# Optimization experiments

Hardware: AMD Instinct MI355X
Metric: run time of the kernel (lower is better)

## Reference

```python
import jax, jax.numpy as jnp
import numpy as np


def bilinear_resize(x, out_h, out_w):
    # x: [B, C, H, W]; matches torch F.interpolate(mode='bilinear', align_corners=False)
    B, C, H, W = x.shape
    ry = jnp.clip((jnp.arange(out_h, dtype=jnp.float32) + 0.5) * (H / out_h) - 0.5, 0.0, H - 1)
    rx = jnp.clip((jnp.arange(out_w, dtype=jnp.float32) + 0.5) * (W / out_w) - 0.5, 0.0, W - 1)
    y0 = jnp.floor(ry).astype(jnp.int32); y1 = jnp.minimum(y0 + 1, H - 1)
    x0 = jnp.floor(rx).astype(jnp.int32); x1 = jnp.minimum(x0 + 1, W - 1)
    wy = (ry - y0)[:, None]  # [out_h,1]
    wx = (rx - x0)[None, :]  # [1,out_w]
    r0 = x[:, :, y0, :]; r1 = x[:, :, y1, :]
    v00 = r0[:, :, :, x0]; v01 = r0[:, :, :, x1]
    v10 = r1[:, :, :, x0]; v11 = r1[:, :, :, x1]
    return (v00 * (1 - wx) + v01 * wx) * (1 - wy) + (v10 * (1 - wx) + v11 * wx) * wy


def setup_inputs() -> dict:
    key0 = jax.random.key(0)
    ks = jax.random.split(key0, 16)
    B, N, C, H = 2, 300, 256, 8
    hw_lvl = np.array([[64, 64], [32, 32], [16, 16]], dtype=np.int64)
    L = int((hw_lvl[:, 0] * hw_lvl[:, 1]).sum())  # 5376
    p = lambda k, sh: (0.02 * jax.random.normal(k, sh, dtype=jnp.float32))
    return {
        'query': jax.random.normal(ks[0], (B, N, C), dtype=jnp.float32),
        'key': jax.random.normal(ks[1], (B, L, C), dtype=jnp.float32),
        'value': jax.random.normal(ks[2], (B, L, C), dtype=jnp.float32),
        'key_padding_mask': jnp.zeros((B, L), dtype=bool),
        'hw_lvl': hw_lvl,
        'Wq': p(ks[3], (C, C)), 'Wk': p(ks[4], (C, C)), 'Wv': p(ks[5], (C, C)),
        'Wp': p(ks[6], (C, C)), 'bp': jnp.zeros((C,), jnp.float32),
        'W1': p(ks[7], (H, H)), 'b1': jnp.zeros((H,), jnp.float32),
        'W2': p(ks[8], (H, H)), 'b2': jnp.zeros((H,), jnp.float32),
        'W3': p(ks[9], (H, H)), 'b3': jnp.zeros((H,), jnp.float32),
        'Wm': p(ks[10], (3 * H, 1)), 'bm': jnp.zeros((1,), jnp.float32),
    }


def reference(query, key, value, key_padding_mask, hw_lvl,
              Wq, Wk, Wv, Wp, bp, W1, b1, W2, b2, W3, b3, Wm, bm):
    hw = np.asarray(hw_lvl)
    h1, wd1 = int(hw[0, 0]), int(hw[0, 1])
    h2, wd2 = int(hw[1, 0]), int(hw[1, 1])
    h3, wd3 = int(hw[2, 0]), int(hw[2, 1])
    w1 = h1 * wd1
    w2 = w1 + h2 * wd2
    B, N, C = query.shape
    L = key.shape[1]
    H = W1.shape[0]
    scale = (C // H) ** -0.5

    q = (query @ Wq).reshape(B, N, H, C // H)
    k = (key @ Wk).reshape(B, L, H, C // H)
    v = (value @ Wv).reshape(B, L, H, C // H)
    attn = jnp.einsum('bnhd,blhd->bhnl', q, k) * scale  # [B,H,N,L]

    ap = attn.transpose(0, 2, 3, 1)  # [B,N,L,H]
    f1 = jax.nn.relu(ap[:, :, :w1] @ W1 + b1)                      # [B,N,w1,H]
    f2 = jax.nn.relu(ap[:, :, w1:w2] @ W2 + b2)                    # [B,N,h2*wd2,H]
    f3 = jax.nn.relu(ap[:, :, w2:] @ W3 + b3)                      # [B,N,h3*wd3,H]
    f2 = f2.transpose(0, 1, 3, 2).reshape(B * N, H, h2, wd2)
    f3 = f3.transpose(0, 1, 3, 2).reshape(B * N, H, h3, wd3)
    f2 = bilinear_resize(f2, h1, wd1).transpose(0, 2, 3, 1).reshape(B, N, w1, H)
    f3 = bilinear_resize(f3, h1, wd1).transpose(0, 2, 3, 1).reshape(B, N, w1, H)
    new_feats = jnp.concatenate([f1, f2, f3], axis=-1)             # [B,N,w1,3H]
    mask = jax.nn.relu(new_feats @ Wm + bm)                        # [B,N,w1,1]

    aw = jax.nn.softmax(attn, axis=-1)                             # [B,H,N,L]
    x = jnp.einsum('bhnl,blhd->bnhd', aw, v).reshape(B, N, C)
    x = x @ Wp + bp
    return x, mask
```

## Files before the change

kernel.cpp:

```cpp
#include <hip/hip_runtime.h>
#include <hip/hip_bf16.h>

typedef __hip_bfloat16 bf16;
typedef __attribute__((ext_vector_type(8))) short short8v;
typedef __attribute__((ext_vector_type(8))) unsigned short ushort8v;
typedef __attribute__((ext_vector_type(4))) unsigned short ushort4v;
typedef __attribute__((ext_vector_type(4))) float float4v;

__device__ __forceinline__ float bfu2f(unsigned short u) {
    union { unsigned int i; float f; } v; v.i = ((unsigned int)u) << 16; return v.f;
}
__device__ __forceinline__ unsigned short f2bfu_rn(float x) {
    union { float f; unsigned int i; } u; u.f = x;
    unsigned int r = (u.i + 0x7FFFu + ((u.i >> 16) & 1u)) >> 16;
    return (unsigned short)r;
}

__global__ __launch_bounds__(256) void cast_wt(
    const float* __restrict__ Wq, const float* __restrict__ Wk,
    const float* __restrict__ Wv, const float* __restrict__ Wp,
    unsigned short* __restrict__ wt)
{
    __shared__ unsigned short tile[64][72];
    const float* W = (blockIdx.z == 0) ? Wq : (blockIdx.z == 1) ? Wk
                   : (blockIdx.z == 2) ? Wv : Wp;
    unsigned short* WT = wt + (size_t)blockIdx.z * 65536;
    const int t = threadIdx.x;
    const int k0 = blockIdx.x * 64, n0 = blockIdx.y * 64;
    {
        const int r = t >> 2, cseg = (t & 3) * 16;
        const float* src = W + (size_t)(k0 + r) * 256 + n0 + cseg;
        #pragma unroll
        for (int j = 0; j < 16; ++j) tile[r][cseg + j] = f2bfu_rn(src[j]);
    }
    __syncthreads();
    {
        const int ch = t & 63, lq = t >> 6;
        ushort8v o0, o1;
        #pragma unroll
        for (int i = 0; i < 8; ++i) o0[i] = tile[lq * 16 + i][ch];
        #pragma unroll
        for (int i = 0; i < 8; ++i) o1[i] = tile[lq * 16 + 8 + i][ch];
        unsigned short* dst = WT + (size_t)(n0 + ch) * 256 + k0 + lq * 16;
        *(ushort8v*)(dst)     = o0;
        *(ushort8v*)(dst + 8) = o1;
    }
}

__device__ __forceinline__ void proj_core(
    const float* __restrict__ aptr, const unsigned short* __restrict__ Wt,
    int nc0, int m16, int quad, float4v acc[8])
{
    #pragma unroll
    for (int i = 0; i < 8; ++i) acc[i] = (float4v){0.f, 0.f, 0.f, 0.f};
    #pragma unroll
    for (int ks = 0; ks < 8; ++ks) {
        float4 a0 = *(const float4*)(aptr + ks * 32);
        float4 a1 = *(const float4*)(aptr + ks * 32 + 4);
        short8v af;
        af[0] = (short)f2bfu_rn(a0.x); af[1] = (short)f2bfu_rn(a0.y);
        af[2] = (short)f2bfu_rn(a0.z); af[3] = (short)f2bfu_rn(a0.w);
        af[4] = (short)f2bfu_rn(a1.x); af[5] = (short)f2bfu_rn(a1.y);
        af[6] = (short)f2bfu_rn(a1.z); af[7] = (short)f2bfu_rn(a1.w);
        #pragma unroll
        for (int i = 0; i < 8; ++i) {
            short8v bfr = *(const short8v*)(Wt + (size_t)(nc0 + i * 16 + m16) * 256 + ks * 32 + quad * 8);
            acc[i] = __builtin_amdgcn_mfma_f32_16x16x32_bf16(af, bfr, acc[i], 0, 0, 0);
        }
    }
}

__global__ __launch_bounds__(256) void proj_all(
    const float* __restrict__ q, const float* __restrict__ k, const float* __restrict__ v,
    const unsigned short* __restrict__ wt,
    unsigned short* __restrict__ qb, unsigned short* __restrict__ kb,
    unsigned short* __restrict__ vt)
{
    const int t = threadIdx.x;
    const int wave = t >> 6, lane = t & 63;
    const int m16 = lane & 15, quad = lane >> 4;
    const int msub = (wave & 1) * 16;
    const int nc0 = (wave >> 1) * 128;
    const int bx = blockIdx.x;

    float4v acc[8];
    if (bx < 19) {
        const int m0 = bx * 32;
        const int arow = min(m0 + msub + m16, 599);
        proj_core(q + (size_t)arow * 256 + quad * 8, wt, nc0, m16, quad, acc);
        #pragma unroll
        for (int i = 0; i < 8; ++i)
            #pragma unroll
            for (int r = 0; r < 4; ++r) {
                int m = m0 + msub + quad * 4 + r;
                if (m < 600)
                    qb[(size_t)m * 256 + nc0 + i * 16 + m16] = f2bfu_rn(acc[i][r]);
            }
    } else if (bx < 355) {
        const int m0 = (bx - 19) * 32;
        proj_core(k + (size_t)(m0 + msub + m16) * 256 + quad * 8, wt + 65536, nc0, m16, quad, acc);
        #pragma unroll
        for (int i = 0; i < 8; ++i)
            #pragma unroll
            for (int r = 0; r < 4; ++r) {
                int m = m0 + msub + quad * 4 + r;
                kb[(size_t)m * 256 + nc0 + i * 16 + m16] = f2bfu_rn(acc[i][r]);
            }
    } else {
        const int m0 = (bx - 355) * 32;
        proj_core(v + (size_t)(m0 + msub + m16) * 256 + quad * 8, wt + 131072, nc0, m16, quad, acc);
        const int bb = (m0 >= 5376) ? 1 : 0;
        const int lcol = m0 - bb * 5376 + msub + quad * 4;
        #pragma unroll
        for (int i = 0; i < 8; ++i) {
            const int ch = nc0 + i * 16 + m16;
            ushort4v p;
            #pragma unroll
            for (int r = 0; r < 4; ++r) p[r] = f2bfu_rn(acc[i][r]);
            *(ushort4v*)(vt + (size_t)(bb * 256 + ch) * 5376 + lcol) = p;
        }
    }
}

__global__ __launch_bounds__(512) void attn_fused(
    const unsigned short* __restrict__ qb, const unsigned short* __restrict__ kb,
    const unsigned short* __restrict__ vt,
    unsigned short* __restrict__ attn, float* __restrict__ xbp, float* __restrict__ Sp)
{
    __shared__ unsigned short probs[8][16 * 236];
    __shared__ float partial[8][64][9];
    __shared__ float SrowP[8][16];

    const int t = threadIdx.x;
    const int wave = t >> 6, lane = t & 63;

    const int i0 = blockIdx.x;
    const int c = i0 & 7;
    int m = i0 >> 3;
    const int half = (m >= 57) ? 1 : 0;
    const int bh = c * 2 + half;
    m -= half * 57;
    const int n0 = (m % 19) * 16;
    const int zz = m / 19;

    const int b = bh >> 3, h = bh & 7;
    const int m16 = lane & 15, quad = lane >> 4;
    const float scale = 0.17677669529663687f;

    const unsigned short* qp = qb + (size_t)(b * 300 + min(n0 + m16, 299)) * 256 + h * 32 + quad * 8;
    const short8v qfrag = *(const short8v*)qp;

    const unsigned short* kbase = kb + (size_t)(b * 5376) * 256 + h * 32 + quad * 8;
    const unsigned short* vt0 = vt + (size_t)(b * 256 + h * 32 + m16) * 5376;
    const unsigned short* vt1 = vt0 + (size_t)16 * 5376;

    unsigned short* pw = &probs[wave][0];
    const int lc = zz * 1792 + wave * 224;

    float4v c0 = {0.f, 0.f, 0.f, 0.f};
    float4v c1 = {0.f, 0.f, 0.f, 0.f};
    float sm = 0.f;

    #pragma unroll
    for (int i = 0; i < 14; ++i) {
        const int lcol = lc + i * 16 + m16;
        short8v kf = *(const short8v*)(kbase + (size_t)lcol * 256);
        float4v c = {0.f, 0.f, 0.f, 0.f};
        c = __builtin_amdgcn_mfma_f32_16x16x32_bf16(kf, qfrag, c, 0, 0, 0);
        ushort4v pk;
        #pragma unroll
        for (int r = 0; r < 4; ++r) pk[r] = f2bfu_rn(c[r] * scale);
        *(ushort4v*)(pw + m16 * 236 + i * 16 + quad * 4) = pk;
    }

    {
        const int row = lane >> 2;
        const int n = n0 + row;
        if (n < 300) {
            unsigned short* gdst = attn + ((size_t)(b * 300 + n) * 8 + h) * 5376 + lc;
            const unsigned short* lsrc = pw + row * 236;
            #pragma unroll
            for (int it = 0; it < 7; ++it) {
                const int colk = (lane & 3) * 8 + it * 32;
                *(ushort8v*)(gdst + colk) = *(const ushort8v*)(lsrc + colk);
            }
        }
    }

    #pragma unroll
    for (int step = 0; step < 7; ++step) {
        const int lloc = step * 32 + quad * 8;
        ushort8v ua = *(const ushort8v*)(pw + m16 * 236 + lloc);
        short8v af;
        #pragma unroll
        for (int j = 0; j < 8; ++j) {
            float e = __expf(bfu2f(ua[j]));
            sm += e;
            af[j] = (short)f2bfu_rn(e);
        }
        const int lg = lc + lloc;
        short8v b0 = *(const short8v*)(vt0 + lg);
        short8v b1 = *(const short8v*)(vt1 + lg);
        c0 = __builtin_amdgcn_mfma_f32_16x16x32_bf16(af, b0, c0, 0, 0, 0);
        c1 = __builtin_amdgcn_mfma_f32_16x16x32_bf16(af, b1, c1, 0, 0, 0);
    }

    sm += __shfl_xor(sm, 16);
    sm += __shfl_xor(sm, 32);
    if (lane < 16) SrowP[wave][lane] = sm;
    #pragma unroll
    for (int j = 0; j < 4; ++j) {
        partial[wave][lane][j]     = c0[j];
        partial[wave][lane][4 + j] = c1[j];
    }
    __syncthreads();

    if (t < 64) {
        float acc[8] = {0.f, 0.f, 0.f, 0.f, 0.f, 0.f, 0.f, 0.f};
        #pragma unroll
        for (int w = 0; w < 8; ++w)
            #pragma unroll
            for (int j = 0; j < 8; ++j) acc[j] += partial[w][t][j];

        const int d = t & 15, q = t >> 4;
        float* xplane = xbp + (size_t)zz * 153600;
        float* splane = Sp + (size_t)zz * 4800;
        #pragma unroll
        for (int r = 0; r < 4; ++r) {
            const int row = q * 4 + r;
            const int nn = n0 + row;
            if (nn < 300) {
                float S = 0.f;
                #pragma unroll
                for (int w = 0; w < 8; ++w) S += SrowP[w][row];
                if (d == 0) splane[(size_t)(b * 300 + nn) * 8 + h] = S;
                float* o = xplane + (size_t)(b * 300 + nn) * 256 + h * 32 + d;
                o[0]  = acc[r];
                o[16] = acc[4 + r];
            }
        }
    }
}

__global__ __launch_bounds__(256) void proj_out(
    const float* __restrict__ xbp, const float* __restrict__ Sp,
    const unsigned short* __restrict__ Wtp,
    const float* __restrict__ bp, float* __restrict__ out)
{
    const int t = threadIdx.x;
    const int wave = t >> 6, lane = t & 63;
    const int m16 = lane & 15, quad = lane >> 4;
    const int msub = (wave & 1) * 16;
    const int nc0 = (wave >> 1) * 128;
    const int m0 = blockIdx.x * 32;

    const int arow = min(m0 + msub + m16, 599);
    const float* a0p = xbp + (size_t)arow * 256 + quad * 8;

    float4v acc[8];
    #pragma unroll
    for (int i = 0; i < 8; ++i) acc[i] = (float4v){0.f, 0.f, 0.f, 0.f};

    #pragma unroll
    for (int ks = 0; ks < 8; ++ks) {
        const float S = Sp[(size_t)arow * 8 + ks]
                      + Sp[4800 + (size_t)arow * 8 + ks]
                      + Sp[9600 + (size_t)arow * 8 + ks];
        const float rS = 1.0f / S;
        float a[8];
        #pragma unroll
        for (int half = 0; half < 2; ++half) {
            const float* p = a0p + ks * 32 + half * 4;
            float4 x0 = *(const float4*)(p);
            float4 x1 = *(const float4*)(p + 153600);
            float4 x2 = *(const float4*)(p + 307200);
            a[half * 4 + 0] = (x0.x + x1.x + x2.x) * rS;
            a[half * 4 + 1] = (x0.y + x1.y + x2.y) * rS;
            a[half * 4 + 2] = (x0.z + x1.z + x2.z) * rS;
            a[half * 4 + 3] = (x0.w + x1.w + x2.w) * rS;
        }
        short8v af;
        #pragma unroll
        for (int j = 0; j < 8; ++j) af[j] = (short)f2bfu_rn(a[j]);
        #pragma unroll
        for (int i = 0; i < 8; ++i) {
            short8v bfr = *(const short8v*)(Wtp + (size_t)(nc0 + i * 16 + m16) * 256 + ks * 32 + quad * 8);
            acc[i] = __builtin_amdgcn_mfma_f32_16x16x32_bf16(af, bfr, acc[i], 0, 0, 0);
        }
    }

    #pragma unroll
    for (int i = 0; i < 8; ++i) {
        const float bv = bp[nc0 + i * 16 + m16];
        #pragma unroll
        for (int r = 0; r < 4; ++r) {
            int m = m0 + msub + quad * 4 + r;
            if (m < 600)
                out[(size_t)m * 256 + nc0 + i * 16 + m16] = acc[i][r] + bv;
        }
    }
}

__global__ __launch_bounds__(256) void gfields_kernel(
    const unsigned short* __restrict__ attn,
    const float* __restrict__ W2, const float* __restrict__ b2,
    const float* __restrict__ W3, const float* __restrict__ b3,
    const float* __restrict__ Wm, float* __restrict__ gf)
{
    __shared__ float w2s[64], w3s[64], b2s[8], b3s[8], wms[24];
    const int t = threadIdx.x;
    const int bn = blockIdx.x;
    const unsigned short* ap = attn + (size_t)bn * 8 * 5376;
    float* g = gf + (size_t)bn * 1280;

    if (t < 64) { w2s[t] = W2[t]; w3s[t] = W3[t]; }
    if (t < 8)  { b2s[t] = b2[t]; b3s[t] = b3[t]; }
    if (t < 24) wms[t] = Wm[t];
    __syncthreads();

    {
        const int l2 = t * 4;
        ushort4v u[8];
        #pragma unroll
        for (int hh = 0; hh < 8; ++hh)
            u[hh] = *(const ushort4v*)(ap + hh * 5376 + 4096 + l2);
        float4 o;
        float* op = (float*)&o;
        #pragma unroll
        for (int pp = 0; pp < 4; ++pp) {
            float gg = 0.f;
            #pragma unroll
            for (int hh = 0; hh < 8; ++hh) {
                float s = b2s[hh];
                #pragma unroll
                for (int hp = 0; hp < 8; ++hp) s += bfu2f(u[hp][pp]) * w2s[hp * 8 + hh];
                gg += fmaxf(s, 0.f) * wms[8 + hh];
            }
            op[pp] = gg;
        }
        *(float4*)(g + l2) = o;
    }
    if (t < 64) {
        const int l3 = t * 4;
        ushort4v u[8];
        #pragma unroll
        for (int hh = 0; hh < 8; ++hh)
            u[hh] = *(const ushort4v*)(ap + hh * 5376 + 5120 + l3);
        float4 o;
        float* op = (float*)&o;
        #pragma unroll
        for (int pp = 0; pp < 4; ++pp) {
            float gg = 0.f;
            #pragma unroll
            for (int hh = 0; hh < 8; ++hh) {
                float s = b3s[hh];
                #pragma unroll
                for (int hp = 0; hp < 8; ++hp) s += bfu2f(u[hp][pp]) * w3s[hp * 8 + hh];
                gg += fmaxf(s, 0.f) * wms[16 + hh];
            }
            op[pp] = gg;
        }
        *(float4*)(g + 1024 + l3) = o;
    }
}

__global__ __launch_bounds__(256) void mask_px(
    const unsigned short* __restrict__ attn, const float* __restrict__ gf,
    const float* __restrict__ W1, const float* __restrict__ b1,
    const float* __restrict__ Wm, const float* __restrict__ bmp,
    float* __restrict__ out)
{
    __shared__ float gs[1280];
    __shared__ float w1s[64], b1s[8], wm1[8];
    __shared__ float bms;

    const int t  = threadIdx.x;
    const int bn = blockIdx.x;
    const int ph = blockIdx.y;
    const unsigned short* ap = attn + (size_t)bn * 8 * 5376;

    if (t < 64) w1s[t] = W1[t];
    if (t < 8)  { b1s[t] = b1[t]; wm1[t] = Wm[t]; }
    if (t == 0) bms = bmp[0];
    {
        const float4* src = (const float4*)(gf + (size_t)bn * 1280);
        ((float4*)gs)[t] = src[t];
        if (t < 64) ((float4*)gs)[256 + t] = src[256 + t];
    }
    __syncthreads();

    {
        const int p0 = ph * 1024 + t * 4;
        ushort4v u[8];
        #pragma unroll
        for (int hh = 0; hh < 8; ++hh)
            u[hh] = *(const ushort4v*)(ap + hh * 5376 + p0);

        float4 res;
        float* rp = (float*)&res;
        #pragma unroll
        for (int pp = 0; pp < 4; ++pp) {
            const int p = p0 + pp;
            const int Y = p >> 6, X = p & 63;

            float acc = bms;
            #pragma unroll
            for (int hh = 0; hh < 8; ++hh) {
                float s = b1s[hh];
                #pragma unroll
                for (int hp = 0; hp < 8; ++hp) s += bfu2f(u[hp][pp]) * w1s[hp * 8 + hh];
                acc += fmaxf(s, 0.f) * wm1[hh];
            }
            {
                float ry = fminf(fmaxf(0.5f * Y - 0.25f, 0.f), 31.f);
                float rx = fminf(fmaxf(0.5f * X - 0.25f, 0.f), 31.f);
                int y0 = (int)ry, x0 = (int)rx;
                int y1 = min(y0 + 1, 31), x1 = min(x0 + 1, 31);
                float wy = ry - (float)y0, wx = rx - (float)x0;
                acc += (gs[y0 * 32 + x0] * (1.f - wx) + gs[y0 * 32 + x1] * wx) * (1.f - wy)
                     + (gs[y1 * 32 + x0] * (1.f - wx) + gs[y1 * 32 + x1] * wx) * wy;
            }
            {
                float ry = fminf(fmaxf(0.25f * Y - 0.375f, 0.f), 15.f);
                float rx = fminf(fmaxf(0.25f * X - 0.375f, 0.f), 15.f);
                int y0 = (int)ry, x0 = (int)rx;
                int y1 = min(y0 + 1, 15), x1 = min(x0 + 1, 15);
                float wy = ry - (float)y0, wx = rx - (float)x0;
                acc += (gs[1024 + y0 * 16 + x0] * (1.f - wx) + gs[1024 + y0 * 16 + x1] * wx) * (1.f - wy)
                     + (gs[1024 + y1 * 16 + x0] * (1.f - wx) + gs[1024 + y1 * 16 + x1] * wx) * wy;
            }
            rp[pp] = fmaxf(acc, 0.f);
        }
        *(float4*)(out + 153600 + (size_t)bn * 4096 + p0) = res;
    }
}

extern "C" void kernel_launch(void* const* d_in, const int* in_sizes, int n_in,
                              void* d_out, int out_size, void* d_ws, size_t ws_size,
                              hipStream_t stream) {
    const float* query = (const float*)d_in[0];
    const float* key   = (const float*)d_in[1];
    const float* value = (const float*)d_in[2];
    const float* Wq = (const float*)d_in[5];
    const float* Wk = (const float*)d_in[6];
    const float* Wv = (const float*)d_in[7];
    const float* Wp = (const float*)d_in[8];
    const float* bp = (const float*)d_in[9];
    const float* W1 = (const float*)d_in[10];
    const float* b1 = (const float*)d_in[11];
    const float* W2 = (const float*)d_in[12];
    const float* b2 = (const float*)d_in[13];
    const float* W3 = (const float*)d_in[14];
    const float* b3 = (const float*)d_in[15];
    const float* Wm = (const float*)d_in[16];
    const float* bm = (const float*)d_in[17];
    float* out = (float*)d_out;

    char* ws = (char*)d_ws;
    unsigned short* wt = (unsigned short*)(ws);
    bf16*  qb   = (bf16*) (ws + 524288);
    bf16*  kb   = (bf16*) (ws + 831488);
    bf16*  vt   = (bf16*) (ws + 6336512);
    bf16*  attn = (bf16*) (ws + 11841536);
    float* xbp  = (float*)(ws + 63451136);
    float* Sp   = (float*)(ws + 65294336);
    float* gf   = (float*)(ws + 65351936);

    cast_wt<<<dim3(4, 4, 4), 256, 0, stream>>>(Wq, Wk, Wv, Wp, wt);

    proj_all<<<691, 256, 0, stream>>>(query, key, value, wt,
        (unsigned short*)qb, (unsigned short*)kb, (unsigned short*)vt);

    attn_fused<<<912, 512, 0, stream>>>(
        (const unsigned short*)qb, (const unsigned short*)kb, (const unsigned short*)vt,
        (unsigned short*)attn, xbp, Sp);

    gfields_kernel<<<600, 256, 0, stream>>>(
        (const unsigned short*)attn, W2, b2, W3, b3, Wm, gf);

    mask_px<<<dim3(600, 4), 256, 0, stream>>>(
        (const unsigned short*)attn, gf, W1, b1, Wm, bm, out);

    proj_out<<<19, 256, 0, stream>>>(xbp, Sp, (const unsigned short*)wt + 196608, bp, out);
}
```

Measured before the change: 203.0 us.

## Fuse per-pixel mask MLP into attention kernel, drop bf16 attn map round-trip

The attention kernel now assigns one head per wave and all 8 heads share a 16-query × 448-key tile, so it can evaluate the per-level 8×8 MLP plus Wm dot product directly from LDS scores. It writes the level-1 mask partials and the level-2/3 g fields instead of materialising the full bf16 attention tensor. This removes the large attn write and its re-read in two follow-up kernels. The mask upsample/add and the output projection are merged into a single 'finish' kernel that reduces 12 partial planes. The cost is extra syncthreads, fewer blocks (456), more partial planes to sum, and scalar scattered stores for the mask.

After: 208.0 us. 1.02x slower.

```diff
diff --git a/kernel.cpp b/kernel.cpp
--- a/kernel.cpp
+++ b/kernel.cpp
@@ -125,313 +125,229 @@
 __global__ __launch_bounds__(512) void attn_fused(
     const unsigned short* __restrict__ qb, const unsigned short* __restrict__ kb,
     const unsigned short* __restrict__ vt,
-    unsigned short* __restrict__ attn, float* __restrict__ xbp, float* __restrict__ Sp)
+    const float* __restrict__ W1, const float* __restrict__ b1,
+    const float* __restrict__ W2, const float* __restrict__ b2,
+    const float* __restrict__ W3, const float* __restrict__ b3,
+    const float* __restrict__ Wm,
+    float* __restrict__ xbp, float* __restrict__ Sp,
+    float* __restrict__ g2, float* __restrict__ g3, float* __restrict__ maskp)
 {
     __shared__ unsigned short probs[8][16 * 236];
-    __shared__ float partial[8][64][9];
-    __shared__ float SrowP[8][16];
+    __shared__ float wls[3][64];
+    __shared__ float bls[3][8], wmls[3][8];
 
     const int t = threadIdx.x;
     const int wave = t >> 6, lane = t & 63;
 
     const int i0 = blockIdx.x;
-    const int c = i0 & 7;
-    int m = i0 >> 3;
-    const int half = (m >= 57) ? 1 : 0;
-    const int bh = c * 2 + half;
-    m -= half * 57;
-    const int n0 = (m % 19) * 16;
-    const int zz = m / 19;
-
-    const int b = bh >> 3, h = bh & 7;
+    const int m = (i0 & 7) * 57 + (i0 >> 3);
+    const int grp = m / 19, nt = m % 19;
+    const int b = grp / 12, zz = grp % 12;
+    const int n0 = nt * 16;
+    const int l0 = zz * 448;
+
+    if (t < 64) { wls[0][t] = W1[t]; wls[1][t] = W2[t]; wls[2][t] = W3[t]; }
+    if (t < 8)  { bls[0][t] = b1[t]; bls[1][t] = b2[t]; bls[2][t] = b3[t];
+                  wmls[0][t] = Wm[t]; wmls[1][t] = Wm[8 + t]; wmls[2][t] = Wm[16 + t]; }
+
     const int m16 = lane & 15, quad = lane >> 4;
+    const int h = wave;
     const float scale = 0.17677669529663687f;
 
     const unsigned short* qp = qb + (size_t)(b * 300 + min(n0 + m16, 299)) * 256 + h * 32 + quad * 8;
     const short8v qfrag = *(const short8v*)qp;
-
     const unsigned short* kbase = kb + (size_t)(b * 5376) * 256 + h * 32 + quad * 8;
     const unsigned short* vt0 = vt + (size_t)(b * 256 + h * 32 + m16) * 5376;
     const unsigned short* vt1 = vt0 + (size_t)16 * 5376;
-
     unsigned short* pw = &probs[wave][0];
-    const int lc = zz * 1792 + wave * 224;
 
     float4v c0 = {0.f, 0.f, 0.f, 0.f};
     float4v c1 = {0.f, 0.f, 0.f, 0.f};
     float sm = 0.f;
 
-    #pragma unroll
-    for (int i = 0; i < 14; ++i) {
-        const int lcol = lc + i * 16 + m16;
-        short8v kf = *(const short8v*)(kbase + (size_t)lcol * 256);
-        float4v c = {0.f, 0.f, 0.f, 0.f};
-        c = __builtin_amdgcn_mfma_f32_16x16x32_bf16(kf, qfrag, c, 0, 0, 0);
-        ushort4v pk;
-        #pragma unroll
-        for (int r = 0; r < 4; ++r) pk[r] = f2bfu_rn(c[r] * scale);
-        *(ushort4v*)(pw + m16 * 236 + i * 16 + quad * 4) = pk;
-    }
-
-    {
-        const int row = lane >> 2;
-        const int n = n0 + row;
-        if (n < 300) {
-            unsigned short* gdst = attn + ((size_t)(b * 300 + n) * 8 + h) * 5376 + lc;
-            const unsigned short* lsrc = pw + row * 236;
-            #pragma unroll
-            for (int it = 0; it < 7; ++it) {
-                const int colk = (lane & 3) * 8 + it * 32;
-                *(ushort8v*)(gdst + colk) = *(const ushort8v*)(lsrc + colk);
-            }
-        }
-    }
-
-    #pragma unroll
-    for (int step = 0; step < 7; ++step) {
-        const int lloc = step * 32 + quad * 8;
-        ushort8v ua = *(const ushort8v*)(pw + m16 * 236 + lloc);
-        short8v af;
-        #pragma unroll
-        for (int j = 0; j < 8; ++j) {
-            float e = __expf(bfu2f(ua[j]));
-            sm += e;
-            af[j] = (short)f2bfu_rn(e);
-        }
-        const int lg = lc + lloc;
-        short8v b0 = *(const short8v*)(vt0 + lg);
-        short8v b1 = *(const short8v*)(vt1 + lg);
-        c0 = __builtin_amdgcn_mfma_f32_16x16x32_bf16(af, b0, c0, 0, 0, 0);
-        c1 = __builtin_amdgcn_mfma_f32_16x16x32_bf16(af, b1, c1, 0, 0, 0);
+    for (int sc = 0; sc < 2; ++sc) {
+        const int lc = l0 + sc * 224;
+
+        #pragma unroll
+        for (int i = 0; i < 14; ++i) {
+            const int lcol = lc + i * 16 + m16;
+            short8v kf = *(const short8v*)(kbase + (size_t)lcol * 256);
+            float4v c = {0.f, 0.f, 0.f, 0.f};
+            c = __builtin_amdgcn_mfma_f32_16x16x32_bf16(kf, qfrag, c, 0, 0, 0);
+            ushort4v pk;
+            #pragma unroll
+            for (int r = 0; r < 4; ++r) pk[r] = f2bfu_rn(c[r] * scale);
+            *(ushort4v*)(pw + m16 * 236 + i * 16 + quad * 4) = pk;
+        }
+        __syncthreads();
+
+        {
+            const int nl = t >> 5;
+            const int n = n0 + nl;
+            if (n < 300) {
+                const int lb = (t & 31) * 7;
+                const size_t bn = (size_t)(b * 300 + n);
+                #pragma unroll
+                for (int j = 0; j < 7; ++j) {
+                    const int ll = lb + j;
+                    const int p = lc + ll;
+                    const int lvl = (p >= 4096) + (p >= 5120);
+                    float s[8];
+                    #pragma unroll
+                    for (int hp = 0; hp < 8; ++hp) s[hp] = bfu2f(probs[hp][nl * 236 + ll]);
+                    float acc = 0.f;
+                    #pragma unroll
+                    for (int hh = 0; hh < 8; ++hh) {
+                        float f = bls[lvl][hh];
+                        #pragma unroll
+                        for (int hp = 0; hp < 8; ++hp) f += s[hp] * wls[lvl][hp * 8 + hh];
+                        acc += fmaxf(f, 0.f) * wmls[lvl][hh];
+                    }
+                    if (lvl == 0)      maskp[bn * 4096 + p] = acc;
+                    else if (lvl == 1) g2[bn * 1024 + (p - 4096)] = acc;
+                    else               g3[bn * 256 + (p - 5120)] = acc;
+                }
+            }
+        }
+
+        #pragma unroll
+        for (int step = 0; step < 7; ++step) {
+            const int lloc = step * 32 + quad * 8;
+            ushort8v ua = *(const ushort8v*)(pw + m16 * 236 + lloc);
+            short8v af;
+            #pragma unroll
+            for (int j = 0; j < 8; ++j) {
+                float e = __expf(bfu2f(ua[j]));
+                sm += e;
+                af[j] = (short)f2bfu_rn(e);
+            }
+            const int lg = lc + lloc;
+            short8v bb0 = *(const short8v*)(vt0 + lg);
+            short8v bb1 = *(const short8v*)(vt1 + lg);
+            c0 = __builtin_amdgcn_mfma_f32_16x16x32_bf16(af, bb0, c0, 0, 0, 0);
+            c1 = __builtin_amdgcn_mfma_f32_16x16x32_bf16(af, bb1, c1, 0, 0, 0);
+        }
+        __syncthreads();
     }
 
     sm += __shfl_xor(sm, 16);
     sm += __shfl_xor(sm, 32);
-    if (lane < 16) SrowP[wave][lane] = sm;
+    float* xplane = xbp + (size_t)zz * 153600;
+    float* splane = Sp + (size_t)zz * 4800;
+    if (lane < 16 && n0 + lane < 300)
+        splane[(size_t)(b * 300 + n0 + lane) * 8 + h] = sm;
     #pragma unroll
-    for (int j = 0; j < 4; ++j) {
-        partial[wave][lane][j]     = c0[j];
-        partial[wave][lane][4 + j] = c1[j];
-    }
-    __syncthreads();
-
-    if (t < 64) {
-        float acc[8] = {0.f, 0.f, 0.f, 0.f, 0.f, 0.f, 0.f, 0.f};
-        #pragma unroll
-        for (int w = 0; w < 8; ++w)
-            #pragma unroll
-            for (int j = 0; j < 8; ++j) acc[j] += partial[w][t][j];
-
-        const int d = t & 15, q = t >> 4;
-        float* xplane = xbp + (size_t)zz * 153600;
-        float* splane = Sp + (size_t)zz * 4800;
-        #pragma unroll
-        for (int r = 0; r < 4; ++r) {
-            const int row = q * 4 + r;
-            const int nn = n0 + row;
-            if (nn < 300) {
-                float S = 0.f;
-                #pragma unroll
-                for (int w = 0; w < 8; ++w) S += SrowP[w][row];
-                if (d == 0) splane[(size_t)(b * 300 + nn) * 8 + h] = S;
-                float* o = xplane + (size_t)(b * 300 + nn) * 256 + h * 32 + d;
-                o[0]  = acc[r];
-                o[16] = acc[4 + r];
-            }
-        }
-    }
-}
-
-__global__ __launch_bounds__(256) void proj_out(
+    for (int r = 0; r < 4; ++r) {
+        const int n = n0 + quad * 4 + r;
+        if (n < 300) {
+            float* o = xplane + (size_t)(b * 300 + n) * 256 + h * 32 + m16;
+            o[0]  = c0[r];
+            o[16] = c1[r];
+        }
+    }
+}
+
+__global__ __launch_bounds__(256) void finish(
+    const float* __restrict__ g2, const float* __restrict__ g3,
     const float* __restrict__ xbp, const float* __restrict__ Sp,
     const unsigned short* __restrict__ Wtp,
-    const float* __restrict__ bp, float* __restrict__ out)
+    const float* __restrict__ bpv, const float* __restrict__ bmp,
+    float* __restrict__ out)
 {
     const int t = threadIdx.x;
-    const int wave = t >> 6, lane = t & 63;
-    const int m16 = lane & 15, quad = lane >> 4;
-    const int msub = (wave & 1) * 16;
-    const int nc0 = (wave >> 1) * 128;
-    const int m0 = blockIdx.x * 32;
-
-    const int arow = min(m0 + msub + m16, 599);
-    const float* a0p = xbp + (size_t)arow * 256 + quad * 8;
-
-    float4v acc[8];
-    #pragma unroll
-    for (int i = 0; i < 8; ++i) acc[i] = (float4v){0.f, 0.f, 0.f, 0.f};
-
-    #pragma unroll
-    for (int ks = 0; ks < 8; ++ks) {
-        const float S = Sp[(size_t)arow * 8 + ks]
-                      + Sp[4800 + (size_t)arow * 8 + ks]
-                      + Sp[9600 + (size_t)arow * 8 + ks];
-        const float rS = 1.0f / S;
-        float a[8];
-        #pragma unroll
-        for (int half = 0; half < 2; ++half) {
-            const float* p = a0p + ks * 32 + half * 4;
-            float4 x0 = *(const float4*)(p);
-            float4 x1 = *(const float4*)(p + 153600);
-            float4 x2 = *(const float4*)(p + 307200);
-            a[half * 4 + 0] = (x0.x + x1.x + x2.x) * rS;
-            a[half * 4 + 1] = (x0.y + x1.y + x2.y) * rS;
-            a[half * 4 + 2] = (x0.z + x1.z + x2.z) * rS;
-            a[half * 4 + 3] = (x0.w + x1.w + x2.w) * rS;
-        }
-        short8v af;
-        #pragma unroll
-        for (int j = 0; j < 8; ++j) af[j] = (short)f2bfu_rn(a[j]);
-        #pragma unroll
-        for (int i = 0; i < 8; ++i) {
-            short8v bfr = *(const short8v*)(Wtp + (size_t)(nc0 + i * 16 + m16) * 256 + ks * 32 + quad * 8);
-            acc[i] = __builtin_amdgcn_mfma_f32_16x16x32_bf16(af, bfr, acc[i], 0, 0, 0);
-        }
-    }
-
-    #pragma unroll
-    for (int i = 0; i < 8; ++i) {
-        const float bv = bp[nc0 + i * 16 + m16];
-        #pragma unroll
-        for (int r = 0; r < 4; ++r) {
-            int m = m0 + msub + quad * 4 + r;
-            if (m < 600)
-                out[(size_t)m * 256 + nc0 + i * 16 + m16] = acc[i][r] + bv;
-        }
-    }
-}
-
-__global__ __launch_bounds__(256) void gfields_kernel(
-    const unsigned short* __restrict__ attn,
-    const float* __restrict__ W2, const float* __restrict__ b2,
-    const float* __restrict__ W3, const float* __restrict__ b3,
-    const float* __restrict__ Wm, float* __restrict__ gf)
-{
-    __shared__ float w2s[64], w3s[64], b2s[8], b3s[8], wms[24];
-    const int t = threadIdx.x;
-    const int bn = blockIdx.x;
-    const unsigned short* ap = attn + (size_t)bn * 8 * 5376;
-    float* g = gf + (size_t)bn * 1280;
-
-    if (t < 64) { w2s[t] = W2[t]; w3s[t] = W3[t]; }
-    if (t < 8)  { b2s[t] = b2[t]; b3s[t] = b3[t]; }
-    if (t < 24) wms[t] = Wm[t];
-    __syncthreads();
-
-    {
-        const int l2 = t * 4;
-        ushort4v u[8];
-        #pragma unroll
-        for (int hh = 0; hh < 8; ++hh)
-            u[hh] = *(const ushort4v*)(ap + hh * 5376 + 4096 + l2);
-        float4 o;
-        float* op = (float*)&o;
-        #pragma unroll
-        for (int pp = 0; pp < 4; ++pp) {
-            float gg = 0.f;
-            #pragma unroll
-            for (int hh = 0; hh < 8; ++hh) {
-                float s = b2s[hh];
+    if (blockIdx.x < 600) {
+        __shared__ float gs[1280];
+        __shared__ float bms;
+        const int bn = blockIdx.x;
+        if (t == 0) bms = bmp[0];
+        ((float4v*)gs)[t] = ((const float4v*)(g2 + (size_t)bn * 1024))[t];
+        if (t < 64) ((float4v*)(gs + 1024))[t] = ((const float4v*)(g3 + (size_t)bn * 256))[t];
+        __syncthreads();
+
+        float* mp = out + 153600 + (size_t)bn * 4096;
+        #pragma unroll
+        for (int it = 0; it < 4; ++it) {
+            const int p0 = it * 1024 + t * 4;
+            float4v mv = *(const float4v*)(mp + p0);
+            float4v res;
+            #pragma unroll
+            for (int pp = 0; pp < 4; ++pp) {
+                const int p = p0 + pp;
+                const int Y = p >> 6, X = p & 63;
+                float acc = mv[pp] + bms;
+                {
+                    float ry = fminf(fmaxf(0.5f * Y - 0.25f, 0.f), 31.f);
+                    float rx = fminf(fmaxf(0.5f * X - 0.25f, 0.f), 31.f);
+                    int y0 = (int)ry, x0 = (int)rx;
+                    int y1 = min(y0 + 1, 31), x1 = min(x0 + 1, 31);
+                    float wy = ry - (float)y0, wx = rx - (float)x0;
+                    acc += (gs[y0 * 32 + x0] * (1.f - wx) + gs[y0 * 32 + x1] * wx) * (1.f - wy)
+                         + (gs[y1 * 32 + x0] * (1.f - wx) + gs[y1 * 32 + x1] * wx) * wy;
+                }
+                {
+                    float ry = fminf(fmaxf(0.25f * Y - 0.375f, 0.f), 15.f);
+                    float rx = fminf(fmaxf(0.25f * X - 0.375f, 0.f), 15.f);
+                    int y0 = (int)ry, x0 = (int)rx;
+                    int y1 = min(y0 + 1, 15), x1 = min(x0 + 1, 15);
+                    float wy = ry - (float)y0, wx = rx - (float)x0;
+                    acc += (gs[1024 + y0 * 16 + x0] * (1.f - wx) + gs[1024 + y0 * 16 + x1] * wx) * (1.f - wy)
+                         + (gs[1024 + y1 * 16 + x0] * (1.f - wx) + gs[1024 + y1 * 16 + x1] * wx) * wy;
+            }
+                res[pp] = fmaxf(acc, 0.f);
+            }
+            *(float4v*)(mp + p0) = res;
+        }
+    } else {
+        const int bx = blockIdx.x - 600;
+        const int wave = t >> 6, lane = t & 63;
+        const int m16 = lane & 15, quad = lane >> 4;
+        const int nc0 = wave * 64;
+        const int m0 = bx * 16;
+        const int arow = min(m0 + m16, 599);
+        const float* a0p = xbp + (size_t)arow * 256 + quad * 8;
+
+        float4v acc[4];
+        #pragma unroll
+        for (int i = 0; i < 4; ++i) acc[i] = (float4v){0.f, 0.f, 0.f, 0.f};
+
+        #pragma unroll
+        for (int ks = 0; ks < 8; ++ks) {
+            float S = 0.f;
+            #pragma unroll
+            for (int z = 0; z < 12; ++z) S += Sp[(size_t)z * 4800 + arow * 8 + ks];
+            const float rS = 1.0f / S;
+            float a[8];
+            #pragma unroll
+            for (int half = 0; half < 2; ++half) {
+                float4v x = {0.f, 0.f, 0.f, 0.f};
                 #pragma unroll
-                for (int hp = 0; hp < 8; ++hp) s += bfu2f(u[hp][pp]) * w2s[hp * 8 + hh];
-                gg += fmaxf(s, 0.f) * wms[8 + hh];
-            }
-            op[pp] = gg;
-        }
-        *(float4*)(g + l2) = o;
-    }
-    if (t < 64) {
-        const int l3 = t * 4;
-        ushort4v u[8];
-        #pragma unroll
-        for (int hh = 0; hh < 8; ++hh)
-            u[hh] = *(const ushort4v*)(ap + hh * 5376 + 5120 + l3);
-        float4 o;
-        float* op = (float*)&o;
-        #pragma unroll
-        for (int pp = 0; pp < 4; ++pp) {
-            float gg = 0.f;
-            #pragma unroll
-            for (int hh = 0; hh < 8; ++hh) {
-                float s = b3s[hh];
-                #pragma unroll
-                for (int hp = 0; hp < 8; ++hp) s += bfu2f(u[hp][pp]) * w3s[hp * 8 + hh];
-                gg += fmaxf(s, 0.f) * wms[16 + hh];
-            }
-            op[pp] = gg;
-        }
-        *(float4*)(g + 1024 + l3) = o;
-    }
-}
-
-__global__ __launch_bounds__(256) void mask_px(
-    const unsigned short* __restrict__ attn, const float* __restrict__ gf,
-    const float* __restrict__ W1, const float* __restrict__ b1,
-    const float* __restrict__ Wm, const float* __restrict__ bmp,
-    float* __restrict__ out)
-{
-    __shared__ float gs[1280];
-    __shared__ float w1s[64], b1s[8], wm1[8];
-    __shared__ float bms;
-
-    const int t  = threadIdx.x;
-    const int bn = blockIdx.x;
-    const int ph = blockIdx.y;
-    const unsigned short* ap = attn + (size_t)bn * 8 * 5376;
-
-    if (t < 64) w1s[t] = W1[t];
-    if (t < 8)  { b1s[t] = b1[t]; wm1[t] = Wm[t]; }
-    if (t == 0) bms = bmp[0];
-    {
-        const float4* src = (const float4*)(gf + (size_t)bn * 1280);
-        ((float4*)gs)[t] = src[t];
-        if (t < 64) ((float4*)gs)[256 + t] = src[256 + t];
-    }
-    __syncthreads();
-
-    {
-        const int p0 = ph * 1024 + t * 4;
-        ushort4v u[8];
-        #pragma unroll
-        for (int hh = 0; hh < 8; ++hh)
-            u[hh] = *(const ushort4v*)(ap + hh * 5376 + p0);
-
-        float4 res;
-        float* rp = (float*)&res;
-        #pragma unroll
-        for (int pp = 0; pp < 4; ++pp) {
-            const int p = p0 + pp;
-            const int Y = p >> 6, X = p & 63;
-
-            float acc = bms;
-            #pragma unroll
-            for (int hh = 0; hh < 8; ++hh) {
-                float s = b1s[hh];
-                #pragma unroll
-                for (int hp = 0; hp < 8; ++hp) s += bfu2f(u[hp][pp]) * w1s[hp * 8 + hh];
-                acc += fmaxf(s, 0.f) * wm1[hh];
-            }
-            {
-                float ry = fminf(fmaxf(0.5f * Y - 0.25f, 0.f), 31.f);
-                float rx = fminf(fmaxf(0.5f * X - 0.25f, 0.f), 31.f);
-                int y0 = (int)ry, x0 = (int)rx;
-                int y1 = min(y0 + 1, 31), x1 = min(x0 + 1, 31);
-                float wy = ry - (float)y0, wx = rx - (float)x0;
-                acc += (gs[y0 * 32 + x0] * (1.f - wx) + gs[y0 * 32 + x1] * wx) * (1.f - wy)
-                     + (gs[y1 * 32 + x0] * (1.f - wx) + gs[y1 * 32 + x1] * wx) * wy;
-            }
-            {
-                float ry = fminf(fmaxf(0.25f * Y - 0.375f, 0.f), 15.f);
-                float rx = fminf(fmaxf(0.25f * X - 0.375f, 0.f), 15.f);
-                int y0 = (int)ry, x0 = (int)rx;
-                int y1 = min(y0 + 1, 15), x1 = min(x0 + 1, 15);
-                float wy = ry - (float)y0, wx = rx - (float)x0;
-                acc += (gs[1024 + y0 * 16 + x0] * (1.f - wx) + gs[1024 + y0 * 16 + x1] * wx) * (1.f - wy)
-                     + (gs[1024 + y1 * 16 + x0] * (1.f - wx) + gs[1024 + y1 * 16 + x1] * wx) * wy;
-            }
-            rp[pp] = fmaxf(acc, 0.f);
-        }
-        *(float4*)(out + 153600 + (size_t)bn * 4096 + p0) = res;
+                for (int z = 0; z < 12; ++z)
+                    x += *(const float4v*)(a0p + (size_t)z * 153600 + ks * 32 + half * 4);
+                a[half * 4 + 0] = x[0] * rS;
+                a[half * 4 + 1] = x[1] * rS;
+                a[half * 4 + 2] = x[2] * rS;
+                a[half * 4 + 3] = x[3] * rS;
+            }
+            short8v af;
+            #pragma unroll
+            for (int j = 0; j < 8; ++j) af[j] = (short)f2bfu_rn(a[j]);
+            #pragma unroll
+            for (int i = 0; i < 4; ++i) {
+                short8v bfr = *(const short8v*)(Wtp + (size_t)(nc0 + i * 16 + m16) * 256 + ks * 32 + quad * 8);
+                acc[i] = __builtin_amdgcn_mfma_f32_16x16x32_bf16(af, bfr, acc[i], 0, 0, 0);
+            }
+        }
+
+        #pragma unroll
+        for (int i = 0; i < 4; ++i) {
+            const float bv = bpv[nc0 + i * 16 + m16];
+            #pragma unroll
+            for (int r = 0; r < 4; ++r) {
+                int mm = m0 + quad * 4 + r;
+                if (mm < 600)
+                    out[(size_t)mm * 256 + nc0 + i * 16 + m16] = acc[i][r] + bv;
+            }
+        }
     }
 }
 
@@ -461,25 +377,21 @@
     bf16*  qb   = (bf16*) (ws + 524288);
     bf16*  kb   = (bf16*) (ws + 831488);
     bf16*  vt   = (bf16*) (ws + 6336512);
-    bf16*  attn = (bf16*) (ws + 11841536);
-    float* xbp  = (float*)(ws + 63451136);
-    float* Sp   = (float*)(ws + 65294336);
-    float* gf   = (float*)(ws + 65351936);
+    float* xbp  = (float*)(ws + 11841536);
+    float* Sp   = (float*)(ws + 19214336);
+    float* g2   = (float*)(ws + 19444736);
+    float* g3   = (float*)(ws + 21902336);
+    float* maskp = out + 153600;
 
     cast_wt<<<dim3(4, 4, 4), 256, 0, stream>>>(Wq, Wk, Wv, Wp, wt);
 
     proj_all<<<691, 256, 0, stream>>>(query, key, value, wt,
         (unsigned short*)qb, (unsigned short*)kb, (unsigned short*)vt);
 
-    attn_fused<<<912, 512, 0, stream>>>(
+    attn_fused<<<456, 512, 0, stream>>>(
         (const unsigned short*)qb, (const unsigned short*)kb, (const unsigned short*)vt,
-        (unsigned short*)attn, xbp, Sp);
-
-    gfields_kernel<<<600, 256, 0, stream>>>(
-        (const unsigned short*)attn, W2, b2, W3, b3, Wm, gf);
-
-    mask_px<<<dim3(600, 4), 256, 0, stream>>>(
-        (const unsigned short*)attn, gf, W1, b1, Wm, bm, out);
-
-    proj_out<<<19, 256, 0, stream>>>(xbp, Sp, (const unsigned short*)wt + 196608, bp, out);
-}
+        W1, b1, W2, b2, W3, b3, Wm, xbp, Sp, g2, g3, maskp);
+
+    finish<<<638, 256, 0, stream>>>(g2, g3, xbp, Sp,
+        (const unsigned short*)wt + 196608, bp, bm, out);
+}
```
